# Kernel optimization log

Measured on AMD Instinct MI355X. Metric: run time of the kernel, lower is better.

Reference implementation:

```python
import jax, jax.numpy as jnp
import numpy as np

N = 50000      # nodes
E = 800000     # edges (before self-loops)
H = 4          # heads
NEG_SLOPE = 0.2
EPS = 1e-16


def setup_inputs() -> dict:
    key = jax.random.key(0)
    ks = jax.random.split(key, 10)
    m, hidden, m_y = 128, 32, 32
    x = jax.random.normal(ks[0], (N, m), jnp.float32)
    edge_index = jax.random.randint(ks[1], (2, E), 0, N, jnp.int32)
    s1 = 1.0 / np.sqrt(m)
    s2 = 1.0 / np.sqrt(H * hidden)
    W1 = jax.random.normal(ks[2], (m, H * hidden), jnp.float32) * s1
    a1_src = jax.random.normal(ks[3], (H, hidden), jnp.float32) * s1
    a1_dst = jax.random.normal(ks[4], (H, hidden), jnp.float32) * s1
    b1 = jnp.zeros((H * hidden,), jnp.float32)
    W2 = jax.random.normal(ks[5], (H * hidden, H * m_y), jnp.float32) * s2
    a2_src = jax.random.normal(ks[6], (H, m_y), jnp.float32) * s2
    a2_dst = jax.random.normal(ks[7], (H, m_y), jnp.float32) * s2
    b2 = jnp.zeros((H * m_y,), jnp.float32)
    return {"x": x, "edge_index": edge_index, "W1": W1, "a1_src": a1_src,
            "a1_dst": a1_dst, "b1": b1, "W2": W2, "a2_src": a2_src,
            "a2_dst": a2_dst, "b2": b2}


def gat_conv(x, W, a_src, a_dst, bias, src, dst):
    # x: [N, F_in], W: [F_in, H*C]
    C = a_src.shape[1]
    h = (x @ W).reshape(N, H, C)                      # [N, H, C]
    alpha_s = jnp.einsum('nhc,hc->nh', h, a_src)       # [N, H]
    alpha_d = jnp.einsum('nhc,hc->nh', h, a_dst)       # [N, H]
    e = jax.nn.leaky_relu(alpha_s[src] + alpha_d[dst], NEG_SLOPE)  # [Etot, H]
    # segment softmax over incoming edges of each dst node
    e_max = jax.ops.segment_max(e, dst, num_segments=N)            # [N, H]
    e_exp = jnp.exp(e - e_max[dst])
    denom = jax.ops.segment_sum(e_exp, dst, num_segments=N)        # [N, H]
    alpha = e_exp / (denom[dst] + EPS)                             # [Etot, H]
    out = jax.ops.segment_sum(h[src] * alpha[:, :, None], dst, num_segments=N)
    return out.reshape(N, H * C) + bias


def reference(x, edge_index, W1, a1_src, a1_dst, b1, W2, a2_src, a2_dst, b2):
    # add self-loops (PyG GATConv default add_self_loops=True)
    loops = jnp.arange(N, dtype=edge_index.dtype)
    src = jnp.concatenate([edge_index[0], loops])
    dst = jnp.concatenate([edge_index[1], loops])
    out = gat_conv(x, W1, a1_src, a1_dst, b1, src, dst)
    out = jax.nn.elu(out)
    # dropout(p=0.8) is identity in eval mode
    out = gat_conv(out, W2, a2_src, a2_dst, b2, src, dst)
    return out
```

## Files before the change

kernel.cpp:

```cpp
#include <hip/hip_runtime.h>
#include <math.h>
#include <stdint.h>

static __device__ __forceinline__ float lrelu(float x) { return x >= 0.f ? x : 0.2f * x; }

static __device__ __forceinline__ uint32_t f2bf(float f) {
    uint32_t u = __float_as_uint(f);
    return (u + 0x7FFFu + ((u >> 16) & 1u)) >> 16;
}

__global__ __launch_bounds__(256) void count_rank(const int* __restrict__ dst, int E,
                                                  int* __restrict__ deg,
                                                  int* __restrict__ rank) {
    int i = blockIdx.x * 256 + threadIdx.x;
    if (i < E) rank[i] = atomicAdd(&deg[dst[i]], 1);
}

__global__ __launch_bounds__(256) void scan1(const int* __restrict__ deg, int N, int ntot,
                                             int* __restrict__ rowptr, int* __restrict__ csum) {
    __shared__ int s[256];
    int t = threadIdx.x;
    int i = blockIdx.x * 256 + t;
    int v = (i < N) ? ((deg[i] + 15) & ~15) : 0;
    s[t] = v;
    __syncthreads();
    #pragma unroll
    for (int off = 1; off < 256; off <<= 1) {
        int add = (t >= off) ? s[t - off] : 0;
        __syncthreads();
        s[t] += add;
        __syncthreads();
    }
    if (i < ntot) rowptr[i] = s[t] - v;
    if (t == 255) csum[blockIdx.x] = s[255];
}

__global__ __launch_bounds__(256) void scan2(const int* __restrict__ csum,
                                             int* __restrict__ coff, int nch) {
    __shared__ int s[256];
    int t = threadIdx.x;
    int v = (t < nch) ? csum[t] : 0;
    s[t] = v;
    __syncthreads();
    #pragma unroll
    for (int off = 1; off < 256; off <<= 1) {
        int add = (t >= off) ? s[t - off] : 0;
        __syncthreads();
        s[t] += add;
        __syncthreads();
    }
    coff[t] = s[t] - v;
}

__global__ __launch_bounds__(256) void scan3(int* __restrict__ rowptr,
                                             const int* __restrict__ coff, int ntot) {
    int i = blockIdx.x * 256 + threadIdx.x;
    if (i < ntot) rowptr[i] += coff[blockIdx.x];
}

__global__ __launch_bounds__(256) void pad_fill(const int* __restrict__ deg,
                                                const int* __restrict__ rowptr,
                                                int* __restrict__ colidx,
                                                float* __restrict__ as_,
                                                uint32_t* __restrict__ hbf, int N) {
    int i = blockIdx.x * 256 + threadIdx.x;
    if (i < 4) as_[N * 4 + i] = -1e30f;
    if (i < 64) hbf[(size_t)N * 64 + i] = 0u;
    if (i < N) {
        int b = rowptr[i] + deg[i];
        int e = rowptr[i + 1];
        for (int p = b; p < e; ++p) colidx[p] = N;
    }
}

__global__ __launch_bounds__(256) void fill_csr(const int* __restrict__ src,
                                                const int* __restrict__ dst,
                                                const int* __restrict__ rank, int E,
                                                const int* __restrict__ rowptr,
                                                int* __restrict__ colidx) {
    int i = blockIdx.x * 256 + threadIdx.x;
    if (i < E) colidx[rowptr[dst[i]] + rank[i]] = src[i];
}

__global__ __launch_bounds__(256) void gemm_alpha(const float* __restrict__ x,
                                                  const float* __restrict__ W,
                                                  const float* __restrict__ a_src,
                                                  const float* __restrict__ a_dst,
                                                  uint32_t* __restrict__ hbf,
                                                  float* __restrict__ as_,
                                                  float* __restrict__ ad_,
                                                  int nrows) {
    __shared__ float xs[128 * 32];
    __shared__ float ws[32 * 128];
    const int t = threadIdx.x;
    const int row0 = blockIdx.x * 128;
    const int rg = t >> 4;
    const int cg = t & 15;
    const int r0 = rg * 8;
    const int c0 = cg * 8;

    float acc[8][8];
    #pragma unroll
    for (int j = 0; j < 8; ++j)
        #pragma unroll
        for (int c = 0; c < 8; ++c) acc[j][c] = 0.f;

    const float4* x4 = (const float4*)x;
    const float4* W4 = (const float4*)W;
    float4* xs4 = (float4*)xs;
    float4* ws4 = (float4*)ws;

    for (int kc = 0; kc < 4; ++kc) {
        #pragma unroll
        for (int i = 0; i < 4; ++i) {
            int idx = t + i * 256;
            int r = idx >> 3, q = idx & 7;
            float4 v = make_float4(0.f, 0.f, 0.f, 0.f);
            if (row0 + r < nrows) v = x4[(size_t)(row0 + r) * 32 + kc * 8 + q];
            xs4[idx] = v;
        }
        #pragma unroll
        for (int i = 0; i < 4; ++i) {
            int idx = t + i * 256;
            int kk2 = idx >> 5, q = idx & 31;
            int dq = (q & 1) ? (16 + (q >> 1)) : (q >> 1);
            ws4[kk2 * 32 + dq] = W4[kc * 1024 + idx];
        }
        __syncthreads();

        #pragma unroll 2
        for (int kk = 0; kk < 32; kk += 4) {
            float4 xv[8];
            #pragma unroll
            for (int j = 0; j < 8; ++j)
                xv[j] = xs4[(r0 + j) * 8 + (kk >> 2)];
            #pragma unroll
            for (int k2 = 0; k2 < 4; ++k2) {
                int k = kk + k2;
                float4 wv0 = ws4[k * 32 + cg];
                float4 wv1 = ws4[k * 32 + 16 + cg];
                #pragma unroll
                for (int j = 0; j < 8; ++j) {
                    float xk = (k2 == 0) ? xv[j].x : (k2 == 1) ? xv[j].y
                             : (k2 == 2) ? xv[j].z : xv[j].w;
                    acc[j][0] = fmaf(xk, wv0.x, acc[j][0]);
                    acc[j][1] = fmaf(xk, wv0.y, acc[j][1]);
                    acc[j][2] = fmaf(xk, wv0.z, acc[j][2]);
                    acc[j][3] = fmaf(xk, wv0.w, acc[j][3]);
                    acc[j][4] = fmaf(xk, wv1.x, acc[j][4]);
                    acc[j][5] = fmaf(xk, wv1.y, acc[j][5]);
                    acc[j][6] = fmaf(xk, wv1.z, acc[j][6]);
                    acc[j][7] = fmaf(xk, wv1.w, acc[j][7]);
                }
            }
        }
        __syncthreads();
    }

    const int hd = cg >> 2;
    float asv[8], adv[8];
    #pragma unroll
    for (int cc = 0; cc < 8; ++cc) {
        asv[cc] = a_src[c0 + cc];
        adv[cc] = a_dst[c0 + cc];
    }
    #pragma unroll
    for (int j = 0; j < 8; ++j) {
        int r = row0 + r0 + j;
        float ps = 0.f, pd = 0.f;
        #pragma unroll
        for (int cc = 0; cc < 8; ++cc) {
            ps = fmaf(acc[j][cc], asv[cc], ps);
            pd = fmaf(acc[j][cc], adv[cc], pd);
        }
        ps += __shfl_xor(ps, 1); ps += __shfl_xor(ps, 2);
        pd += __shfl_xor(pd, 1); pd += __shfl_xor(pd, 2);
        if (r < nrows) {
            uint4 pk;
            pk.x = f2bf(acc[j][0]) | (f2bf(acc[j][1]) << 16);
            pk.y = f2bf(acc[j][2]) | (f2bf(acc[j][3]) << 16);
            pk.z = f2bf(acc[j][4]) | (f2bf(acc[j][5]) << 16);
            pk.w = f2bf(acc[j][6]) | (f2bf(acc[j][7]) << 16);
            *(uint4*)&hbf[(size_t)r * 64 + cg * 4] = pk;
            if ((cg & 3) == 0) {
                as_[r * 4 + hd] = ps;
                ad_[r * 4 + hd] = pd;
            }
        }
    }
}

__global__ __launch_bounds__(256) void aggregate(const uint32_t* __restrict__ hb,
                                                 const float* __restrict__ as_,
                                                 const float* __restrict__ ad_,
                                                 const int* __restrict__ rowptr,
                                                 const int* __restrict__ colidx,
                                                 const float* __restrict__ bias,
                                                 float* __restrict__ out, int n, int do_elu) {
    int node = blockIdx.x * 4 + (threadIdx.x >> 6);
    if (node >= n) return;
    int lane = threadIdx.x & 63;
    int hd = lane >> 4;
    int k = lane * 2;
    int ce = lane >> 2;
    int ch = lane & 3;
    float adn = ad_[node * 4 + hd];
    float adc = ad_[node * 4 + ch];
    float accx = 0.f, accy = 0.f, denom = 0.f;

    {
        float wgt = __expf(lrelu(as_[node * 4 + hd] + adn));
        uint32_t u = hb[(size_t)node * 64 + lane];
        accx = fmaf(wgt, __uint_as_float(u << 16), accx);
        accy = fmaf(wgt, __uint_as_float(u & 0xFFFF0000u), accy);
        denom += wgt;
    }
    const int beg = rowptr[node], end = rowptr[node + 1];
    for (int j = beg; j < end; j += 16) {
        int sE[16];
        #pragma unroll
        for (int e = 0; e < 16; ++e) sE[e] = colidx[j + e];
        int sw = colidx[j + ce];
        float aw = as_[sw * 4 + ch];
        uint32_t u[16];
        #pragma unroll
        for (int e = 0; e < 16; ++e) u[e] = hb[(size_t)sE[e] * 64 + lane];
        float w = __expf(lrelu(aw + adc));
        #pragma unroll
        for (int e = 0; e < 16; ++e) {
            float we = __shfl(w, e * 4 + hd);
            accx = fmaf(we, __uint_as_float(u[e] << 16), accx);
            accy = fmaf(we, __uint_as_float(u[e] & 0xFFFF0000u), accy);
            denom += we;
        }
    }
    float inv = 1.f / (denom + 1e-16f);
    float o0 = fmaf(accx, inv, bias[k]);
    float o1 = fmaf(accy, inv, bias[k + 1]);
    if (do_elu) {
        o0 = o0 > 0.f ? o0 : (__expf(o0) - 1.f);
        o1 = o1 > 0.f ? o1 : (__expf(o1) - 1.f);
    }
    *(float2*)&out[(size_t)node * 128 + k] = make_float2(o0, o1);
}

extern "C" void kernel_launch(void* const* d_in, const int* in_sizes, int n_in,
                              void* d_out, int out_size, void* d_ws, size_t ws_size,
                              hipStream_t stream) {
    const float* x   = (const float*)d_in[0];
    const int*   ei  = (const int*)d_in[1];
    const float* W1  = (const float*)d_in[2];
    const float* a1s = (const float*)d_in[3];
    const float* a1d = (const float*)d_in[4];
    const float* b1  = (const float*)d_in[5];
    const float* W2  = (const float*)d_in[6];
    const float* a2s = (const float*)d_in[7];
    const float* a2d = (const float*)d_in[8];
    const float* b2  = (const float*)d_in[9];
    float* out = (float*)d_out;

    const int N = in_sizes[0] / 128;
    const int E = in_sizes[1] / 2;
    const int* esrc = ei;
    const int* edst = ei + E;

    char* w = (char*)d_ws;
    uint32_t* hbf  = (uint32_t*)w; w += (size_t)(N + 1) * 64 * 4;
    float*    as_  = (float*)w;    w += (size_t)(N + 1) * 4 * 4;
    float*    ad_  = (float*)w;    w += (size_t)(N + 1) * 4 * 4;
    int* deg    = (int*)w;   w += (size_t)N * 4;
    int* rowptr = (int*)w;   w += (size_t)(N + 1) * 4;
    int* rank   = (int*)w;   w += (size_t)E * 4;
    int* colidx = (int*)w;   w += ((size_t)E + 16ull * N) * 4;
    int* csum   = (int*)w;   w += 256 * 4;
    int* coff   = (int*)w;   w += 256 * 4;
    float* out1 = out;

    hipMemsetAsync(deg, 0, (size_t)N * 4, stream);

    const int eb = (E + 255) / 256;
    const int ntot = N + 1;
    const int nch = (ntot + 255) / 256;
    const int gb = (N + 127) / 128;
    const int nb = (N + 3) / 4;
    const int pb = (N + 255) / 256;

    count_rank<<<eb, 256, 0, stream>>>(edst, E, deg, rank);
    scan1<<<nch, 256, 0, stream>>>(deg, N, ntot, rowptr, csum);
    scan2<<<1, 256, 0, stream>>>(csum, coff, nch);
    scan3<<<nch, 256, 0, stream>>>(rowptr, coff, ntot);
    pad_fill<<<pb, 256, 0, stream>>>(deg, rowptr, colidx, as_, hbf, N);
    fill_csr<<<eb, 256, 0, stream>>>(esrc, edst, rank, E, rowptr, colidx);

    gemm_alpha<<<gb, 256, 0, stream>>>(x, W1, a1s, a1d, hbf, as_, ad_, N);
    aggregate<<<nb, 256, 0, stream>>>(hbf, as_, ad_, rowptr, colidx, b1, out1, N, 1);

    gemm_alpha<<<gb, 256, 0, stream>>>(out1, W2, a2s, a2d, hbf, as_, ad_, N);
    aggregate<<<nb, 256, 0, stream>>>(hbf, as_, ad_, rowptr, colidx, b2, out, N, 0);
}
```

Before: 294.1 us.

## Replace FP32 SIMT GEMM with bf16 MFMA GEMM and fuse CSR fill kernels

The scalar FP32 tiled GEMM that computes h and the attention logits is replaced with a bf16 MFMA kernel (16x16x32) using 64-row tiles. Inputs are converted to bf16 in LDS, and weights are pre-transposed and converted by a small prep kernel. The pad-fill and CSR-fill kernels are merged into one launch to save a launch. The GEMM now rounds its inputs to bf16, which reduces precision, and each call pays for an extra weight-prep kernel.

```diff
diff --git a/kernel.cpp b/kernel.cpp
--- a/kernel.cpp
+++ b/kernel.cpp
@@ -2,11 +2,26 @@
 #include <math.h>
 #include <stdint.h>
 
+typedef __attribute__((ext_vector_type(8))) short short8;
+typedef __attribute__((ext_vector_type(4))) float f32x4;
+
 static __device__ __forceinline__ float lrelu(float x) { return x >= 0.f ? x : 0.2f * x; }
 
 static __device__ __forceinline__ uint32_t f2bf(float f) {
     uint32_t u = __float_as_uint(f);
     return (u + 0x7FFFu + ((u >> 16) & 1u)) >> 16;
+}
+
+__global__ __launch_bounds__(256) void wprep(const float* __restrict__ W1,
+                                             const float* __restrict__ W2,
+                                             uint16_t* __restrict__ wtb1,
+                                             uint16_t* __restrict__ wtb2) {
+    int idx = blockIdx.x * 256 + threadIdx.x;
+    const float* src = (idx < 16384) ? W1 : W2;
+    uint16_t* dst = (idx < 16384) ? wtb1 : wtb2;
+    int j = idx & 16383;
+    int k = j >> 7, col = j & 127;
+    dst[col * 128 + k] = (uint16_t)f2bf(src[j]);
 }
 
 __global__ __launch_bounds__(256) void count_rank(const int* __restrict__ dst, int E,
@@ -58,134 +73,135 @@
     if (i < ntot) rowptr[i] += coff[blockIdx.x];
 }
 
-__global__ __launch_bounds__(256) void pad_fill(const int* __restrict__ deg,
-                                                const int* __restrict__ rowptr,
-                                                int* __restrict__ colidx,
-                                                float* __restrict__ as_,
-                                                uint32_t* __restrict__ hbf, int N) {
-    int i = blockIdx.x * 256 + threadIdx.x;
-    if (i < 4) as_[N * 4 + i] = -1e30f;
-    if (i < 64) hbf[(size_t)N * 64 + i] = 0u;
-    if (i < N) {
-        int b = rowptr[i] + deg[i];
-        int e = rowptr[i + 1];
-        for (int p = b; p < e; ++p) colidx[p] = N;
-    }
-}
-
-__global__ __launch_bounds__(256) void fill_csr(const int* __restrict__ src,
+__global__ __launch_bounds__(256) void fill_pad(const int* __restrict__ src,
                                                 const int* __restrict__ dst,
                                                 const int* __restrict__ rank, int E,
                                                 const int* __restrict__ rowptr,
-                                                int* __restrict__ colidx) {
-    int i = blockIdx.x * 256 + threadIdx.x;
-    if (i < E) colidx[rowptr[dst[i]] + rank[i]] = src[i];
-}
-
-__global__ __launch_bounds__(256) void gemm_alpha(const float* __restrict__ x,
-                                                  const float* __restrict__ W,
-                                                  const float* __restrict__ a_src,
-                                                  const float* __restrict__ a_dst,
-                                                  uint32_t* __restrict__ hbf,
-                                                  float* __restrict__ as_,
-                                                  float* __restrict__ ad_,
-                                                  int nrows) {
-    __shared__ float xs[128 * 32];
-    __shared__ float ws[32 * 128];
+                                                const int* __restrict__ deg,
+                                                int* __restrict__ colidx,
+                                                float* __restrict__ as_,
+                                                uint32_t* __restrict__ hbf, int N, int eb) {
+    if ((int)blockIdx.x < eb) {
+        int i = blockIdx.x * 256 + threadIdx.x;
+        if (i < E) colidx[rowptr[dst[i]] + rank[i]] = src[i];
+    } else {
+        int i = (blockIdx.x - eb) * 256 + threadIdx.x;
+        if (i < 4) as_[N * 4 + i] = -1e30f;
+        if (i < 64) hbf[(size_t)N * 64 + i] = 0u;
+        if (i < N) {
+            int b = rowptr[i] + deg[i];
+            int e = rowptr[i + 1];
+            for (int p = b; p < e; ++p) colidx[p] = N;
+        }
+    }
+}
+
+__global__ __launch_bounds__(256) void gemm_mfma(const float* __restrict__ x,
+                                                 const uint16_t* __restrict__ wtb,
+                                                 const float* __restrict__ a_src,
+                                                 const float* __restrict__ a_dst,
+                                                 uint32_t* __restrict__ hbf,
+                                                 float* __restrict__ as_,
+                                                 float* __restrict__ ad_,
+                                                 int nrows) {
+    __shared__ __align__(16) char lds[52224];
     const int t = threadIdx.x;
-    const int row0 = blockIdx.x * 128;
-    const int rg = t >> 4;
-    const int cg = t & 15;
-    const int r0 = rg * 8;
-    const int c0 = cg * 8;
-
-    float acc[8][8];
-    #pragma unroll
-    for (int j = 0; j < 8; ++j)
-        #pragma unroll
-        for (int c = 0; c < 8; ++c) acc[j][c] = 0.f;
-
-    const float4* x4 = (const float4*)x;
-    const float4* W4 = (const float4*)W;
-    float4* xs4 = (float4*)xs;
-    float4* ws4 = (float4*)ws;
-
+    const int row0 = blockIdx.x * 64;
+
+    {
+        int r = t >> 2;
+        int k16b = (t & 3) * 4;
+        const float* xrow = x + (size_t)(row0 + r) * 128;
+        bool ok = (row0 + r) < nrows;
+        #pragma unroll
+        for (int i = 0; i < 4; ++i) {
+            int k16 = k16b + i;
+            float4 va = make_float4(0.f, 0.f, 0.f, 0.f), vb = va;
+            if (ok) {
+                va = *(const float4*)(xrow + k16 * 8);
+                vb = *(const float4*)(xrow + k16 * 8 + 4);
+            }
+            uint4 pk;
+            pk.x = f2bf(va.x) | (f2bf(va.y) << 16);
+            pk.y = f2bf(va.z) | (f2bf(va.w) << 16);
+            pk.z = f2bf(vb.x) | (f2bf(vb.y) << 16);
+            pk.w = f2bf(vb.z) | (f2bf(vb.w) << 16);
+            *(uint4*)(lds + r * 272 + k16 * 16) = pk;
+        }
+    }
+    {
+        #pragma unroll
+        for (int i = 0; i < 8; ++i) {
+            int u = t * 8 + i;
+            int col = u >> 4, k16 = u & 15;
+            uint4 v = *(const uint4*)(wtb + col * 128 + k16 * 8);
+            *(uint4*)(lds + 17408 + col * 272 + k16 * 16) = v;
+        }
+    }
+    __syncthreads();
+
+    const int w = t >> 6, lane = t & 63;
+    const int wrow0 = w * 16;
+    const int la = lane & 15, lb = lane >> 4;
+
+    f32x4 acc[8];
+    #pragma unroll
+    for (int ct = 0; ct < 8; ++ct) acc[ct] = (f32x4){0.f, 0.f, 0.f, 0.f};
+
+    const char* xsb = lds + (wrow0 + la) * 272;
+    const char* wsb = lds + 17408;
+    #pragma unroll
     for (int kc = 0; kc < 4; ++kc) {
-        #pragma unroll
-        for (int i = 0; i < 4; ++i) {
-            int idx = t + i * 256;
-            int r = idx >> 3, q = idx & 7;
-            float4 v = make_float4(0.f, 0.f, 0.f, 0.f);
-            if (row0 + r < nrows) v = x4[(size_t)(row0 + r) * 32 + kc * 8 + q];
-            xs4[idx] = v;
-        }
-        #pragma unroll
-        for (int i = 0; i < 4; ++i) {
-            int idx = t + i * 256;
-            int kk2 = idx >> 5, q = idx & 31;
-            int dq = (q & 1) ? (16 + (q >> 1)) : (q >> 1);
-            ws4[kk2 * 32 + dq] = W4[kc * 1024 + idx];
-        }
-        __syncthreads();
-
-        #pragma unroll 2
-        for (int kk = 0; kk < 32; kk += 4) {
-            float4 xv[8];
+        int k16 = kc * 4 + lb;
+        short8 a = *(const short8*)(xsb + k16 * 16);
+        #pragma unroll
+        for (int ct = 0; ct < 8; ++ct) {
+            int col = ct * 16 + la;
+            short8 b = *(const short8*)(wsb + col * 272 + k16 * 16);
+            acc[ct] = __builtin_amdgcn_mfma_f32_16x16x32_bf16(a, b, acc[ct], 0, 0, 0);
+        }
+    }
+    __syncthreads();
+
+    float* scr = (float*)lds;
+    #pragma unroll
+    for (int ct = 0; ct < 8; ++ct)
+        #pragma unroll
+        for (int r2 = 0; r2 < 4; ++r2)
+            scr[(wrow0 + lb * 4 + r2) * 132 + ct * 16 + la] = acc[ct][r2];
+    __syncthreads();
+
+    {
+        int row = t >> 2, q = t & 3;
+        int grow = row0 + row;
+        float v[32];
+        #pragma unroll
+        for (int m = 0; m < 8; ++m) {
+            float4 f = *(const float4*)(scr + row * 132 + q * 32 + m * 4);
+            v[m * 4 + 0] = f.x; v[m * 4 + 1] = f.y;
+            v[m * 4 + 2] = f.z; v[m * 4 + 3] = f.w;
+        }
+        if (grow < nrows) {
+            uint32_t* orow = hbf + (size_t)grow * 64 + q * 16;
             #pragma unroll
-            for (int j = 0; j < 8; ++j)
-                xv[j] = xs4[(r0 + j) * 8 + (kk >> 2)];
+            for (int m2 = 0; m2 < 4; ++m2) {
+                uint4 pk;
+                pk.x = f2bf(v[m2 * 8 + 0]) | (f2bf(v[m2 * 8 + 1]) << 16);
+                pk.y = f2bf(v[m2 * 8 + 2]) | (f2bf(v[m2 * 8 + 3]) << 16);
+                pk.z = f2bf(v[m2 * 8 + 4]) | (f2bf(v[m2 * 8 + 5]) << 16);
+                pk.w = f2bf(v[m2 * 8 + 6]) | (f2bf(v[m2 * 8 + 7]) << 16);
+                *(uint4*)(orow + m2 * 4) = pk;
+            }
+            float ps = 0.f, pd = 0.f;
+            const float* asp = a_src + q * 32;
+            const float* adp = a_dst + q * 32;
             #pragma unroll
-            for (int k2 = 0; k2 < 4; ++k2) {
-                int k = kk + k2;
-                float4 wv0 = ws4[k * 32 + cg];
-                float4 wv1 = ws4[k * 32 + 16 + cg];
-                #pragma unroll
-                for (int j = 0; j < 8; ++j) {
-                    float xk = (k2 == 0) ? xv[j].x : (k2 == 1) ? xv[j].y
-                             : (k2 == 2) ? xv[j].z : xv[j].w;
-                    acc[j][0] = fmaf(xk, wv0.x, acc[j][0]);
-                    acc[j][1] = fmaf(xk, wv0.y, acc[j][1]);
-                    acc[j][2] = fmaf(xk, wv0.z, acc[j][2]);
-                    acc[j][3] = fmaf(xk, wv0.w, acc[j][3]);
-                    acc[j][4] = fmaf(xk, wv1.x, acc[j][4]);
-                    acc[j][5] = fmaf(xk, wv1.y, acc[j][5]);
-                    acc[j][6] = fmaf(xk, wv1.z, acc[j][6]);
-                    acc[j][7] = fmaf(xk, wv1.w, acc[j][7]);
-                }
+            for (int j = 0; j < 32; ++j) {
+                ps = fmaf(v[j], asp[j], ps);
+                pd = fmaf(v[j], adp[j], pd);
             }
-        }
-        __syncthreads();
-    }
-
-    const int hd = cg >> 2;
-    float asv[8], adv[8];
-    #pragma unroll
-    for (int cc = 0; cc < 8; ++cc) {
-        asv[cc] = a_src[c0 + cc];
-        adv[cc] = a_dst[c0 + cc];
-    }
-    #pragma unroll
-    for (int j = 0; j < 8; ++j) {
-        int r = row0 + r0 + j;
-        float ps = 0.f, pd = 0.f;
-        #pragma unroll
-        for (int cc = 0; cc < 8; ++cc) {
-            ps = fmaf(acc[j][cc], asv[cc], ps);
-            pd = fmaf(acc[j][cc], adv[cc], pd);
-        }
-        ps += __shfl_xor(ps, 1); ps += __shfl_xor(ps, 2);
-        pd += __shfl_xor(pd, 1); pd += __shfl_xor(pd, 2);
-        if (r < nrows) {
-            uint4 pk;
-            pk.x = f2bf(acc[j][0]) | (f2bf(acc[j][1]) << 16);
-            pk.y = f2bf(acc[j][2]) | (f2bf(acc[j][3]) << 16);
-            pk.z = f2bf(acc[j][4]) | (f2bf(acc[j][5]) << 16);
-            pk.w = f2bf(acc[j][6]) | (f2bf(acc[j][7]) << 16);
-            *(uint4*)&hbf[(size_t)r * 64 + cg * 4] = pk;
-            if ((cg & 3) == 0) {
-                as_[r * 4 + hd] = ps;
-                ad_[r * 4 + hd] = pd;
-            }
+            as_[grow * 4 + q] = ps;
+            ad_[grow * 4 + q] = pd;
         }
     }
 }
@@ -274,6 +290,8 @@
     int* colidx = (int*)w;   w += ((size_t)E + 16ull * N) * 4;
     int* csum   = (int*)w;   w += 256 * 4;
     int* coff   = (int*)w;   w += 256 * 4;
+    uint16_t* wtb1 = (uint16_t*)w; w += 16384 * 2;
+    uint16_t* wtb2 = (uint16_t*)w; w += 16384 * 2;
     float* out1 = out;
 
     hipMemsetAsync(deg, 0, (size_t)N * 4, stream);
@@ -281,20 +299,21 @@
     const int eb = (E + 255) / 256;
     const int ntot = N + 1;
     const int nch = (ntot + 255) / 256;
-    const int gb = (N + 127) / 128;
+    const int gb = (N + 63) / 64;
     const int nb = (N + 3) / 4;
     const int pb = (N + 255) / 256;
 
+    wprep<<<128, 256, 0, stream>>>(W1, W2, wtb1, wtb2);
     count_rank<<<eb, 256, 0, stream>>>(edst, E, deg, rank);
     scan1<<<nch, 256, 0, stream>>>(deg, N, ntot, rowptr, csum);
     scan2<<<1, 256, 0, stream>>>(csum, coff, nch);
     scan3<<<nch, 256, 0, stream>>>(rowptr, coff, ntot);
-    pad_fill<<<pb, 256, 0, stream>>>(deg, rowptr, colidx, as_, hbf, N);
-    fill_csr<<<eb, 256, 0, stream>>>(esrc, edst, rank, E, rowptr, colidx);
-
-    gemm_alpha<<<gb, 256, 0, stream>>>(x, W1, a1s, a1d, hbf, as_, ad_, N);
+    fill_pad<<<eb + pb, 256, 0, stream>>>(esrc, edst, rank, E, rowptr, deg,
+                                          colidx, as_, hbf, N, eb);
+
+    gemm_mfma<<<gb, 256, 0, stream>>>(x, wtb1, a1s, a1d, hbf, as_, ad_, N);
     aggregate<<<nb, 256, 0, stream>>>(hbf, as_, ad_, rowptr, colidx, b1, out1, N, 1);
 
-    gemm_alpha<<<gb, 256, 0, stream>>>(out1, W2, a2s, a2d, hbf, as_, ad_, N);
+    gemm_mfma<<<gb, 256, 0, stream>>>(out1, wtb2, a2s, a2d, hbf, as_, ad_, N);
     aggregate<<<nb, 256, 0, stream>>>(hbf, as_, ad_, rowptr, colidx, b2, out, N, 0);
 }
```

Result: faster. 269.1 us (-8.5%).
